# Kernel tuning notes

Hardware: AMD Instinct MI355X
Metric: run time of the kernel (lower is better)

## Reference

```python
import jax, jax.numpy as jnp
import numpy as np

NW, NT, ND = 100000, 10000, 50000
D = 128
E = {"ww": 200000, "wt": 100000, "wd": 150000, "td": 100000, "tt": 50000}


def setup_inputs() -> dict:
    key = jax.random.key(0)
    ks = iter(jax.random.split(key, 40))
    inp = {
        "h_word": jax.random.normal(next(ks), (NW, D), dtype=jnp.float32),
        "h_topic": jax.random.normal(next(ks), (NT, D), dtype=jnp.float32),
        "h_doc": jax.random.normal(next(ks), (ND, D), dtype=jnp.float32),
    }
    for et in ["ww", "wt", "wd", "td", "tt"]:
        inp[f"W_{et}"] = jax.random.normal(next(ks), (D, D), dtype=jnp.float32) * 0.05
        inp[f"b_{et}"] = jax.random.normal(next(ks), (D,), dtype=jnp.float32) * 0.05
    sizes = {"ww": (NW, NW), "wt": (NW, NT), "wd": (NW, ND), "td": (NT, ND), "tt": (NT, NT)}
    for et, (ns, nd) in sizes.items():
        inp[f"src_{et}"] = jax.random.randint(next(ks), (E[et],), 0, ns, dtype=jnp.int32)
        inp[f"dst_{et}"] = jax.random.randint(next(ks), (E[et],), 0, nd, dtype=jnp.int32)
        inp[f"ew_{et}"] = jax.random.uniform(next(ks), (E[et],), dtype=jnp.float32)
    return inp


def _linear(x, W, b):
    # torch nn.Linear: y = x @ W.T + b, W is [out, in]
    return x @ W.T + b


def _mean_agg(h_src, src, dst, ew, n_dst):
    # message m_e = h_src[src_e] * ew_e (u_mul_e), then per-dst mean (fn.mean)
    m = h_src[src] * ew[:, None]                               # [E, D]
    s = jax.ops.segment_sum(m, dst, num_segments=n_dst)        # [n_dst, D]
    cnt = jax.ops.segment_sum(jnp.ones_like(ew), dst, num_segments=n_dst)
    return s / jnp.maximum(cnt, 1.0)[:, None]


def reference(h_word, h_topic, h_doc,
              W_ww, b_ww, W_wt, b_wt, W_wd, b_wd, W_td, b_td, W_tt, b_tt,
              src_ww, dst_ww, ew_ww, src_wt, dst_wt, ew_wt,
              src_wd, dst_wd, ew_wd, src_td, dst_td, ew_td,
              src_tt, dst_tt, ew_tt):
    # DGL loop overwrites src node 'h' in-place -> linears COMPOSE per src type,
    # and messages (resolved at multi_update_all) use the final composed 'h'.
    hw = _linear(_linear(_linear(h_word, W_ww, b_ww), W_wt, b_wt), W_wd, b_wd)
    ht = _linear(_linear(h_topic, W_td, b_td), W_tt, b_tt)
    nw, nt, nd = h_word.shape[0], h_topic.shape[0], h_doc.shape[0]
    # cross-relation 'sum' of per-relation means
    out_word = _mean_agg(hw, src_ww, dst_ww, ew_ww, nw)
    out_topic = _mean_agg(hw, src_wt, dst_wt, ew_wt, nt) + _mean_agg(ht, src_tt, dst_tt, ew_tt, nt)
    out_doc = _mean_agg(hw, src_wd, dst_wd, ew_wd, nd) + _mean_agg(ht, src_td, dst_td, ew_td, nd)
    # relu + dropout (eval mode -> identity); concatenate node types for a single output
    return jnp.concatenate([
        jax.nn.relu(out_word), jax.nn.relu(out_topic), jax.nn.relu(out_doc)
    ], axis=0)
```

## Files before the change

### kernel.cpp

```cpp
#include <hip/hip_runtime.h>
#include <hip/hip_bf16.h>

#define DIM 128
#define NWORD 100000
#define NTOPIC 10000
#define NDOC 50000
#define NOUT (NWORD + NTOPIC + NDOC)

#define E_WW 200000
#define E_WT 100000
#define E_WD 150000
#define E_TD 100000
#define E_TT 50000
#define E_TOT 600000

#define B_WW 0
#define B_WT 100000
#define B_TT 110000
#define B_WD 120000
#define B_TD 170000
#define NSLOT 220000
#define NBLK_SCAN 215

typedef __attribute__((ext_vector_type(8))) short bf16x8;
typedef __attribute__((ext_vector_type(8))) unsigned short u16x8;
typedef __attribute__((ext_vector_type(4))) float f32x4;

__device__ __forceinline__ unsigned short f2bf(float f) {
    __hip_bfloat16 h = __float2bfloat16(f);
    return __builtin_bit_cast(unsigned short, h);
}
__device__ __forceinline__ float b2f(unsigned short u) {
    return __builtin_bit_cast(float, (unsigned)u << 16);
}

__global__ void compose1(const float* __restrict__ W_ww, const float* __restrict__ b_ww,
                         const float* __restrict__ W_wt, const float* __restrict__ b_wt,
                         const float* __restrict__ W_wd, const float* __restrict__ b_wd,
                         const float* __restrict__ W_td, const float* __restrict__ b_td,
                         const float* __restrict__ W_tt, const float* __restrict__ b_tt,
                         float* __restrict__ A, unsigned short* __restrict__ Wbf_t,
                         float* __restrict__ tmpb, float* __restrict__ c_t)
{
    int b = blockIdx.x, j = threadIdx.x;
    if (b < 128) {
        float s = 0.f;
        for (int m = 0; m < 128; ++m) s = fmaf(W_wd[b * 128 + m], W_wt[m * 128 + j], s);
        A[b * 128 + j] = s;
    } else if (b < 256) {
        int k = b - 128;
        float s = 0.f;
        for (int m = 0; m < 128; ++m) s = fmaf(W_tt[j * 128 + m], W_td[m * 128 + k], s);
        Wbf_t[j * 128 + k] = f2bf(s);
    } else if (b == 256) {
        float s = b_wt[j];
        for (int m = 0; m < 128; ++m) s = fmaf(W_wt[j * 128 + m], b_ww[m], s);
        tmpb[j] = s;
    } else {
        float s = b_tt[j];
        for (int m = 0; m < 128; ++m) s = fmaf(W_tt[j * 128 + m], b_td[m], s);
        c_t[j] = s;
    }
}

__global__ void compose2(const float* __restrict__ W_ww, const float* __restrict__ W_wd,
                         const float* __restrict__ b_wd, const float* __restrict__ A,
                         const float* __restrict__ tmpb,
                         unsigned short* __restrict__ Wbf_w, float* __restrict__ c_w)
{
    int b = blockIdx.x, j = threadIdx.x;
    if (b < 128) {
        int k = b;
        float s = 0.f;
        for (int m = 0; m < 128; ++m) s = fmaf(A[j * 128 + m], W_ww[m * 128 + k], s);
        Wbf_w[j * 128 + k] = f2bf(s);
    } else {
        float s = b_wd[j];
        for (int m = 0; m < 128; ++m) s = fmaf(W_wd[j * 128 + m], tmpb[m], s);
        c_w[j] = s;
    }
}

__global__ __launch_bounds__(256) void transform_mfma(
    const float* __restrict__ x, const unsigned short* __restrict__ Wbf,
    const float* __restrict__ bias, unsigned short* __restrict__ y, int ntiles)
{
    __shared__ __attribute__((aligned(16))) unsigned short xs_all[4][16 * 128];
    const int tid = threadIdx.x;
    const int wid = tid >> 6, l = tid & 63;
    char* xs = (char*)xs_all[wid];
    const int l15 = l & 15, l4 = l >> 4;

    bf16x8 wf[8][4];
#pragma unroll
    for (int cg = 0; cg < 8; ++cg)
#pragma unroll
        for (int ki = 0; ki < 4; ++ki)
            wf[cg][ki] = *(const bf16x8*)&Wbf[(cg * 16 + l15) * 128 + ki * 32 + l4 * 8];

    float bj[8];
#pragma unroll
    for (int cg = 0; cg < 8; ++cg) bj[cg] = bias[cg * 16 + l15];

    const int row_s = l >> 2, ch = l & 3;

    for (int tile = blockIdx.x * 4 + wid; tile < ntiles; tile += gridDim.x * 4) {
        const size_t rb = (size_t)tile * 16;

        const float* xr = &x[(rb + row_s) * 128 + ch * 32];
#pragma unroll
        for (int c = 0; c < 4; ++c) {
            float4 u = *(const float4*)(xr + c * 8);
            float4 v = *(const float4*)(xr + c * 8 + 4);
            u16x8 p;
            p[0] = f2bf(u.x); p[1] = f2bf(u.y); p[2] = f2bf(u.z); p[3] = f2bf(u.w);
            p[4] = f2bf(v.x); p[5] = f2bf(v.y); p[6] = f2bf(v.z); p[7] = f2bf(v.w);
            int off = row_s * 256 + ((ch * 64 + c * 16) ^ ((row_s & 7) << 4));
            *(u16x8*)(xs + off) = p;
        }

        f32x4 acc[8];
        const f32x4 zero = {0.f, 0.f, 0.f, 0.f};
#pragma unroll
        for (int cg = 0; cg < 8; ++cg) acc[cg] = zero;

#pragma unroll
        for (int ki = 0; ki < 4; ++ki) {
            int aoff = l15 * 256 + ((ki * 64 + l4 * 16) ^ ((l15 & 7) << 4));
            bf16x8 af = *(const bf16x8*)(xs + aoff);
#pragma unroll
            for (int cg = 0; cg < 8; ++cg)
                acc[cg] = __builtin_amdgcn_mfma_f32_16x16x32_bf16(af, wf[cg][ki], acc[cg], 0, 0, 0);
        }

        unsigned short* yr = &y[(rb + l4 * 4) * 128 + l15];
#pragma unroll
        for (int cg = 0; cg < 8; ++cg)
#pragma unroll
            for (int r = 0; r < 4; ++r)
                yr[r * 128 + cg * 16] = f2bf(acc[cg][r] + bj[cg]);
    }
}

__global__ void rank_count(const int* __restrict__ dst_ww, const int* __restrict__ dst_wt,
                           const int* __restrict__ dst_wd, const int* __restrict__ dst_td,
                           const int* __restrict__ dst_tt,
                           unsigned* __restrict__ cnt, unsigned* __restrict__ rank)
{
    int g = blockIdx.x * 256 + threadIdx.x;
    int slotidx;
    if (g < E_WW)                            slotidx = B_WW + dst_ww[g];
    else if (g < E_WW + E_WT)                slotidx = B_WT + dst_wt[g - E_WW];
    else if (g < E_WW + E_WT + E_WD)         slotidx = B_WD + dst_wd[g - E_WW - E_WT];
    else if (g < E_WW + E_WT + E_WD + E_TD)  slotidx = B_TD + dst_td[g - E_WW - E_WT - E_WD];
    else if (g < E_TOT)                      slotidx = B_TT + dst_tt[g - E_WW - E_WT - E_WD - E_TD];
    else return;
    rank[g] = atomicAdd(&cnt[slotidx], 1u);
}

__global__ __launch_bounds__(256) void scanA(const unsigned* __restrict__ cnt,
                                             unsigned* __restrict__ bsum)
{
    __shared__ unsigned sh[256];
    int t = threadIdx.x;
    int base = blockIdx.x * 1024 + t * 4;
    unsigned s = 0;
#pragma unroll
    for (int i = 0; i < 4; ++i) { int idx = base + i; if (idx < NSLOT) s += cnt[idx]; }
    sh[t] = s; __syncthreads();
    for (int o = 128; o > 0; o >>= 1) { if (t < o) sh[t] += sh[t + o]; __syncthreads(); }
    if (t == 0) bsum[blockIdx.x] = sh[0];
}

__global__ __launch_bounds__(256) void scanB(const unsigned* __restrict__ bsum,
                                             unsigned* __restrict__ boff)
{
    __shared__ unsigned sh[256];
    int t = threadIdx.x;
    unsigned v = (t < NBLK_SCAN) ? bsum[t] : 0u;
    sh[t] = v; __syncthreads();
    for (int o = 1; o < 256; o <<= 1) {
        unsigned x = (t >= o) ? sh[t - o] : 0u;
        __syncthreads();
        sh[t] += x;
        __syncthreads();
    }
    if (t < NBLK_SCAN) boff[t] = sh[t] - v;
}

__global__ __launch_bounds__(256) void scanC(const unsigned* __restrict__ cnt,
                                             const unsigned* __restrict__ boff,
                                             unsigned* __restrict__ offs)
{
    __shared__ unsigned sh[256];
    int t = threadIdx.x;
    int base = blockIdx.x * 1024 + t * 4;
    unsigned c[4]; unsigned s = 0;
#pragma unroll
    for (int i = 0; i < 4; ++i) {
        int idx = base + i;
        c[i] = (idx < NSLOT) ? cnt[idx] : 0u;
        s += c[i];
    }
    sh[t] = s; __syncthreads();
    for (int o = 1; o < 256; o <<= 1) {
        unsigned x = (t >= o) ? sh[t - o] : 0u;
        __syncthreads();
        sh[t] += x;
        __syncthreads();
    }
    unsigned run = boff[blockIdx.x] + sh[t] - s;
#pragma unroll
    for (int i = 0; i < 4; ++i) {
        int idx = base + i;
        if (idx < NSLOT) {
            offs[idx] = run;
            run += c[i];
            if (idx == NSLOT - 1) offs[NSLOT] = run;
        }
    }
}

__global__ void place(const int* __restrict__ dst_ww, const int* __restrict__ dst_wt,
                      const int* __restrict__ dst_wd, const int* __restrict__ dst_td,
                      const int* __restrict__ dst_tt,
                      const int* __restrict__ src_ww, const int* __restrict__ src_wt,
                      const int* __restrict__ src_wd, const int* __restrict__ src_td,
                      const int* __restrict__ src_tt,
                      const float* __restrict__ ew_ww, const float* __restrict__ ew_wt,
                      const float* __restrict__ ew_wd, const float* __restrict__ ew_td,
                      const float* __restrict__ ew_tt,
                      const unsigned* __restrict__ offs, const unsigned* __restrict__ rank,
                      uint2* __restrict__ se)
{
    int g = blockIdx.x * 256 + threadIdx.x;
    int slotidx, e; unsigned sv; float wv;
    if (g < E_WW)                            { e = g;                             slotidx = B_WW + dst_ww[e]; sv = src_ww[e]; wv = ew_ww[e]; }
    else if (g < E_WW + E_WT)                { e = g - E_WW;                      slotidx = B_WT + dst_wt[e]; sv = src_wt[e]; wv = ew_wt[e]; }
    else if (g < E_WW + E_WT + E_WD)         { e = g - E_WW - E_WT;               slotidx = B_WD + dst_wd[e]; sv = src_wd[e]; wv = ew_wd[e]; }
    else if (g < E_WW + E_WT + E_WD + E_TD)  { e = g - E_WW - E_WT - E_WD;        slotidx = B_TD + dst_td[e]; sv = src_td[e]; wv = ew_td[e]; }
    else if (g < E_TOT)                      { e = g - E_WW - E_WT - E_WD - E_TD; slotidx = B_TT + dst_tt[e]; sv = src_tt[e]; wv = ew_tt[e]; }
    else return;
    se[offs[slotidx] + rank[g]] = make_uint2(sv, __builtin_bit_cast(unsigned, wv));
}

__device__ __forceinline__ float4 seg_mean_bf(int slot,
                                              const unsigned* __restrict__ offs,
                                              const uint2* __restrict__ se,
                                              const unsigned short* __restrict__ h, int d4)
{
    unsigned off = offs[slot];
    unsigned deg = offs[slot + 1] - off;
    float ax = 0.f, ay = 0.f, az = 0.f, aw = 0.f;
    for (unsigned j = 0; j < deg; j += 4) {
        uint2 r0 = se[off + j];
        uint2 r1 = se[off + j + 1];
        uint2 r2 = se[off + j + 2];
        uint2 r3 = se[off + j + 3];
        unsigned s0 = r0.x;
        float    w0 = __builtin_bit_cast(float, r0.y);
        unsigned s1 = (j + 1 < deg) ? r1.x : 0u;
        float    w1 = (j + 1 < deg) ? __builtin_bit_cast(float, r1.y) : 0.f;
        unsigned s2 = (j + 2 < deg) ? r2.x : 0u;
        float    w2 = (j + 2 < deg) ? __builtin_bit_cast(float, r2.y) : 0.f;
        unsigned s3 = (j + 3 < deg) ? r3.x : 0u;
        float    w3 = (j + 3 < deg) ? __builtin_bit_cast(float, r3.y) : 0.f;
        ushort4 a0 = *(const ushort4*)&h[(size_t)s0 * 128 + d4];
        ushort4 a1 = *(const ushort4*)&h[(size_t)s1 * 128 + d4];
        ushort4 a2 = *(const ushort4*)&h[(size_t)s2 * 128 + d4];
        ushort4 a3 = *(const ushort4*)&h[(size_t)s3 * 128 + d4];
        ax = fmaf(b2f(a0.x), w0, ax); ay = fmaf(b2f(a0.y), w0, ay);
        az = fmaf(b2f(a0.z), w0, az); aw = fmaf(b2f(a0.w), w0, aw);
        ax = fmaf(b2f(a1.x), w1, ax); ay = fmaf(b2f(a1.y), w1, ay);
        az = fmaf(b2f(a1.z), w1, az); aw = fmaf(b2f(a1.w), w1, aw);
        ax = fmaf(b2f(a2.x), w2, ax); ay = fmaf(b2f(a2.y), w2, ay);
        az = fmaf(b2f(a2.z), w2, az); aw = fmaf(b2f(a2.w), w2, aw);
        ax = fmaf(b2f(a3.x), w3, ax); ay = fmaf(b2f(a3.y), w3, ay);
        az = fmaf(b2f(a3.z), w3, az); aw = fmaf(b2f(a3.w), w3, aw);
    }
    float inv = 1.0f / (float)(deg > 1u ? deg : 1u);
    return float4{ax * inv, ay * inv, az * inv, aw * inv};
}

__global__ void gather(const unsigned* __restrict__ offs,
                       const uint2* __restrict__ se,
                       const unsigned short* __restrict__ hw,
                       const unsigned short* __restrict__ ht,
                       float* __restrict__ out)
{
    int g = blockIdx.x * 256 + threadIdx.x;
    int n = g >> 5, d4 = (g & 31) << 2;
    if (n >= NOUT) return;
    float4 r;
    if (n < NWORD) {
        r = seg_mean_bf(B_WW + n, offs, se, hw, d4);
    } else if (n < NWORD + NTOPIC) {
        int i = n - NWORD;
        float4 a = seg_mean_bf(B_WT + i, offs, se, hw, d4);
        float4 b = seg_mean_bf(B_TT + i, offs, se, ht, d4);
        r = float4{a.x + b.x, a.y + b.y, a.z + b.z, a.w + b.w};
    } else {
        int i = n - NWORD - NTOPIC;
        float4 a = seg_mean_bf(B_WD + i, offs, se, hw, d4);
        float4 b = seg_mean_bf(B_TD + i, offs, se, ht, d4);
        r = float4{a.x + b.x, a.y + b.y, a.z + b.z, a.w + b.w};
    }
    r.x = fmaxf(r.x, 0.f); r.y = fmaxf(r.y, 0.f);
    r.z = fmaxf(r.z, 0.f); r.w = fmaxf(r.w, 0.f);
    *reinterpret_cast<float4*>(&out[(size_t)n * 128 + d4]) = r;
}

extern "C" void kernel_launch(void* const* d_in, const int* in_sizes, int n_in,
                              void* d_out, int out_size, void* d_ws, size_t ws_size,
                              hipStream_t stream) {
    const float* h_word  = (const float*)d_in[0];
    const float* h_topic = (const float*)d_in[1];
    const float* W_ww = (const float*)d_in[3];  const float* b_ww = (const float*)d_in[4];
    const float* W_wt = (const float*)d_in[5];  const float* b_wt = (const float*)d_in[6];
    const float* W_wd = (const float*)d_in[7];  const float* b_wd = (const float*)d_in[8];
    const float* W_td = (const float*)d_in[9];  const float* b_td = (const float*)d_in[10];
    const float* W_tt = (const float*)d_in[11]; const float* b_tt = (const float*)d_in[12];
    const int*   src_ww = (const int*)d_in[13]; const int* dst_ww = (const int*)d_in[14];
    const float* ew_ww  = (const float*)d_in[15];
    const int*   src_wt = (const int*)d_in[16]; const int* dst_wt = (const int*)d_in[17];
    const float* ew_wt  = (const float*)d_in[18];
    const int*   src_wd = (const int*)d_in[19]; const int* dst_wd = (const int*)d_in[20];
    const float* ew_wd  = (const float*)d_in[21];
    const int*   src_td = (const int*)d_in[22]; const int* dst_td = (const int*)d_in[23];
    const float* ew_td  = (const float*)d_in[24];
    const int*   src_tt = (const int*)d_in[25]; const int* dst_tt = (const int*)d_in[26];
    const float* ew_tt  = (const float*)d_in[27];

    float* out = (float*)d_out;

    unsigned short* hw_bf = (unsigned short*)d_ws;
    unsigned short* ht_bf = hw_bf + (size_t)NWORD * 128;
    unsigned short* Wbf_w = ht_bf + (size_t)NTOPIC * 128;
    unsigned short* Wbf_t = Wbf_w + 16384;
    float* fbase = (float*)(Wbf_t + 16384);
    float* c_w   = fbase;
    float* c_t   = c_w + 128;
    float* Amat  = c_t + 128;
    float* tmpb  = Amat + 16384;
    uint2* se    = (uint2*)(tmpb + 128);
    unsigned* cnt  = (unsigned*)(se + E_TOT + 4);
    unsigned* offs = cnt + NSLOT;
    unsigned* rank = offs + NSLOT + 1;
    unsigned* bsum = rank + E_TOT;
    unsigned* boff = bsum + 256;

    hipMemsetAsync(cnt, 0, NSLOT * sizeof(unsigned), stream);

    compose1<<<258, 128, 0, stream>>>(W_ww, b_ww, W_wt, b_wt, W_wd, b_wd, W_td, b_td,
                                      W_tt, b_tt, Amat, Wbf_t, tmpb, c_t);
    compose2<<<129, 128, 0, stream>>>(W_ww, W_wd, b_wd, Amat, tmpb, Wbf_w, c_w);

    rank_count<<<(E_TOT + 255) / 256, 256, 0, stream>>>(dst_ww, dst_wt, dst_wd, dst_td, dst_tt,
                                                        cnt, rank);
    scanA<<<NBLK_SCAN, 256, 0, stream>>>(cnt, bsum);
    scanB<<<1, 256, 0, stream>>>(bsum, boff);
    scanC<<<NBLK_SCAN, 256, 0, stream>>>(cnt, boff, offs);
    place<<<(E_TOT + 255) / 256, 256, 0, stream>>>(
        dst_ww, dst_wt, dst_wd, dst_td, dst_tt,
        src_ww, src_wt, src_wd, src_td, src_tt,
        ew_ww, ew_wt, ew_wd, ew_td, ew_tt, offs, rank, se);

    transform_mfma<<<512, 256, 0, stream>>>(h_word,  Wbf_w, c_w, hw_bf, NWORD / 16);
    transform_mfma<<<80,  256, 0, stream>>>(h_topic, Wbf_t, c_t, ht_bf, NTOPIC / 16);

    gather<<<(NOUT * 32 + 255) / 256, 256, 0, stream>>>(offs, se, hw_bf, ht_bf, out);
}
```

Before: 312.2 us.

## Fuse prep kernels, merge word/topic transforms, and prefetch next tile input

Folds the memset of the count array into the first compose kernel and merges rank_count into the second compose kernel, removing two launches. The two transform_mfma launches become one grid that splits blocks between word and topic work. Inside the transform loop, the next tile's fp32 input is loaded into registers before the current tile's MFMAs run, to overlap global loads with compute. The compose loops also gain four independent accumulators for more ILP, at the cost of higher register use and a slightly different fp32 summation order.

```diff
diff --git a/kernel.cpp b/kernel.cpp
--- a/kernel.cpp
+++ b/kernel.cpp
@@ -22,6 +22,9 @@
 #define NSLOT 220000
 #define NBLK_SCAN 215
 
+#define NBW 512
+#define NBT 64
+
 typedef __attribute__((ext_vector_type(8))) short bf16x8;
 typedef __attribute__((ext_vector_type(8))) unsigned short u16x8;
 typedef __attribute__((ext_vector_type(4))) float f32x4;
@@ -34,24 +37,39 @@
     return __builtin_bit_cast(float, (unsigned)u << 16);
 }
 
-__global__ void compose1(const float* __restrict__ W_ww, const float* __restrict__ b_ww,
-                         const float* __restrict__ W_wt, const float* __restrict__ b_wt,
-                         const float* __restrict__ W_wd, const float* __restrict__ b_wd,
-                         const float* __restrict__ W_td, const float* __restrict__ b_td,
-                         const float* __restrict__ W_tt, const float* __restrict__ b_tt,
-                         float* __restrict__ A, unsigned short* __restrict__ Wbf_t,
-                         float* __restrict__ tmpb, float* __restrict__ c_t)
+__global__ __launch_bounds__(128) void prep1(
+    const float* __restrict__ W_ww, const float* __restrict__ b_ww,
+    const float* __restrict__ W_wt, const float* __restrict__ b_wt,
+    const float* __restrict__ W_wd, const float* __restrict__ b_wd,
+    const float* __restrict__ W_td, const float* __restrict__ b_td,
+    const float* __restrict__ W_tt, const float* __restrict__ b_tt,
+    float* __restrict__ A, unsigned short* __restrict__ Wbf_t,
+    float* __restrict__ tmpb, float* __restrict__ c_t, unsigned* __restrict__ cnt)
 {
     int b = blockIdx.x, j = threadIdx.x;
+    for (int i = b * 128 + j; i < NSLOT; i += gridDim.x * 128) cnt[i] = 0u;
+
     if (b < 128) {
-        float s = 0.f;
-        for (int m = 0; m < 128; ++m) s = fmaf(W_wd[b * 128 + m], W_wt[m * 128 + j], s);
-        A[b * 128 + j] = s;
+        const float* wr = &W_wd[b * 128];
+        float s0 = 0.f, s1 = 0.f, s2 = 0.f, s3 = 0.f;
+        for (int m = 0; m < 128; m += 4) {
+            s0 = fmaf(wr[m + 0], W_wt[(m + 0) * 128 + j], s0);
+            s1 = fmaf(wr[m + 1], W_wt[(m + 1) * 128 + j], s1);
+            s2 = fmaf(wr[m + 2], W_wt[(m + 2) * 128 + j], s2);
+            s3 = fmaf(wr[m + 3], W_wt[(m + 3) * 128 + j], s3);
+        }
+        A[b * 128 + j] = (s0 + s1) + (s2 + s3);
     } else if (b < 256) {
         int k = b - 128;
-        float s = 0.f;
-        for (int m = 0; m < 128; ++m) s = fmaf(W_tt[j * 128 + m], W_td[m * 128 + k], s);
-        Wbf_t[j * 128 + k] = f2bf(s);
+        const float* wr = &W_tt[j * 128];
+        float s0 = 0.f, s1 = 0.f, s2 = 0.f, s3 = 0.f;
+        for (int m = 0; m < 128; m += 4) {
+            s0 = fmaf(wr[m + 0], W_td[(m + 0) * 128 + k], s0);
+            s1 = fmaf(wr[m + 1], W_td[(m + 1) * 128 + k], s1);
+            s2 = fmaf(wr[m + 2], W_td[(m + 2) * 128 + k], s2);
+            s3 = fmaf(wr[m + 3], W_td[(m + 3) * 128 + k], s3);
+        }
+        Wbf_t[j * 128 + k] = f2bf((s0 + s1) + (s2 + s3));
     } else if (b == 256) {
         float s = b_wt[j];
         for (int m = 0; m < 128; ++m) s = fmaf(W_wt[j * 128 + m], b_ww[m], s);
@@ -63,27 +81,52 @@
     }
 }
 
-__global__ void compose2(const float* __restrict__ W_ww, const float* __restrict__ W_wd,
-                         const float* __restrict__ b_wd, const float* __restrict__ A,
-                         const float* __restrict__ tmpb,
-                         unsigned short* __restrict__ Wbf_w, float* __restrict__ c_w)
-{
-    int b = blockIdx.x, j = threadIdx.x;
-    if (b < 128) {
-        int k = b;
-        float s = 0.f;
-        for (int m = 0; m < 128; ++m) s = fmaf(A[j * 128 + m], W_ww[m * 128 + k], s);
-        Wbf_w[j * 128 + k] = f2bf(s);
+__global__ __launch_bounds__(256) void prep2(
+    const float* __restrict__ W_ww, const float* __restrict__ W_wd,
+    const float* __restrict__ b_wd, const float* __restrict__ A,
+    const float* __restrict__ tmpb,
+    unsigned short* __restrict__ Wbf_w, float* __restrict__ c_w,
+    const int* __restrict__ dst_ww, const int* __restrict__ dst_wt,
+    const int* __restrict__ dst_wd, const int* __restrict__ dst_td,
+    const int* __restrict__ dst_tt,
+    unsigned* __restrict__ cnt, unsigned* __restrict__ rank)
+{
+    int b = blockIdx.x, tid = threadIdx.x;
+    if (b < 64) {
+        int k = b * 2 + (tid >> 7), j = tid & 127;
+        const float* ar = &A[j * 128];
+        float s0 = 0.f, s1 = 0.f, s2 = 0.f, s3 = 0.f;
+        for (int m = 0; m < 128; m += 4) {
+            s0 = fmaf(ar[m + 0], W_ww[(m + 0) * 128 + k], s0);
+            s1 = fmaf(ar[m + 1], W_ww[(m + 1) * 128 + k], s1);
+            s2 = fmaf(ar[m + 2], W_ww[(m + 2) * 128 + k], s2);
+            s3 = fmaf(ar[m + 3], W_ww[(m + 3) * 128 + k], s3);
+        }
+        Wbf_w[j * 128 + k] = f2bf((s0 + s1) + (s2 + s3));
+    } else if (b == 64) {
+        if (tid < 128) {
+            float s = b_wd[tid];
+            for (int m = 0; m < 128; ++m) s = fmaf(W_wd[tid * 128 + m], tmpb[m], s);
+            c_w[tid] = s;
+        }
     } else {
-        float s = b_wd[j];
-        for (int m = 0; m < 128; ++m) s = fmaf(W_wd[j * 128 + m], tmpb[m], s);
-        c_w[j] = s;
+        int g = (b - 65) * 256 + tid;
+        int slotidx;
+        if (g < E_WW)                            slotidx = B_WW + dst_ww[g];
+        else if (g < E_WW + E_WT)                slotidx = B_WT + dst_wt[g - E_WW];
+        else if (g < E_WW + E_WT + E_WD)         slotidx = B_WD + dst_wd[g - E_WW - E_WT];
+        else if (g < E_WW + E_WT + E_WD + E_TD)  slotidx = B_TD + dst_td[g - E_WW - E_WT - E_WD];
+        else if (g < E_TOT)                      slotidx = B_TT + dst_tt[g - E_WW - E_WT - E_WD - E_TD];
+        else return;
+        rank[g] = atomicAdd(&cnt[slotidx], 1u);
     }
 }
 
 __global__ __launch_bounds__(256) void transform_mfma(
-    const float* __restrict__ x, const unsigned short* __restrict__ Wbf,
-    const float* __restrict__ bias, unsigned short* __restrict__ y, int ntiles)
+    const float* __restrict__ xw, const unsigned short* __restrict__ Wbf_w,
+    const float* __restrict__ cw, unsigned short* __restrict__ yw, int ntw,
+    const float* __restrict__ xt, const unsigned short* __restrict__ Wbf_t,
+    const float* __restrict__ ct, unsigned short* __restrict__ yt, int ntt)
 {
     __shared__ __attribute__((aligned(16))) unsigned short xs_all[4][16 * 128];
     const int tid = threadIdx.x;
@@ -91,6 +134,15 @@
     char* xs = (char*)xs_all[wid];
     const int l15 = l & 15, l4 = l >> 4;
 
+    const bool isw = blockIdx.x < NBW;
+    const float* x = isw ? xw : xt;
+    const unsigned short* Wbf = isw ? Wbf_w : Wbf_t;
+    const float* bias = isw ? cw : ct;
+    unsigned short* y = isw ? yw : yt;
+    const int nt = isw ? ntw : ntt;
+    const int t0 = (isw ? blockIdx.x : blockIdx.x - NBW) * 4 + wid;
+    const int tstr = (isw ? NBW : NBT) * 4;
+
     bf16x8 wf[8][4];
 #pragma unroll
     for (int cg = 0; cg < 8; ++cg)
@@ -104,19 +156,27 @@
 
     const int row_s = l >> 2, ch = l & 3;
 
-    for (int tile = blockIdx.x * 4 + wid; tile < ntiles; tile += gridDim.x * 4) {
-        const size_t rb = (size_t)tile * 16;
-
-        const float* xr = &x[(rb + row_s) * 128 + ch * 32];
+    float4 u[4], v[4];
+    if (t0 < nt) {
+        const float* xr = &x[((size_t)t0 * 16 + row_s) * 128 + ch * 32];
+#pragma unroll
+        for (int c = 0; c < 4; ++c) { u[c] = *(const float4*)(xr + c * 8); v[c] = *(const float4*)(xr + c * 8 + 4); }
+    }
+
+    for (int tile = t0; tile < nt; tile += tstr) {
 #pragma unroll
         for (int c = 0; c < 4; ++c) {
-            float4 u = *(const float4*)(xr + c * 8);
-            float4 v = *(const float4*)(xr + c * 8 + 4);
             u16x8 p;
-            p[0] = f2bf(u.x); p[1] = f2bf(u.y); p[2] = f2bf(u.z); p[3] = f2bf(u.w);
-            p[4] = f2bf(v.x); p[5] = f2bf(v.y); p[6] = f2bf(v.z); p[7] = f2bf(v.w);
+            p[0] = f2bf(u[c].x); p[1] = f2bf(u[c].y); p[2] = f2bf(u[c].z); p[3] = f2bf(u[c].w);
+            p[4] = f2bf(v[c].x); p[5] = f2bf(v[c].y); p[6] = f2bf(v[c].z); p[7] = f2bf(v[c].w);
             int off = row_s * 256 + ((ch * 64 + c * 16) ^ ((row_s & 7) << 4));
             *(u16x8*)(xs + off) = p;
+        }
+        int nxt = tile + tstr;
+        if (nxt < nt) {
+            const float* xr = &x[((size_t)nxt * 16 + row_s) * 128 + ch * 32];
+#pragma unroll
+            for (int c = 0; c < 4; ++c) { u[c] = *(const float4*)(xr + c * 8); v[c] = *(const float4*)(xr + c * 8 + 4); }
         }
 
         f32x4 acc[8];
@@ -133,29 +193,13 @@
                 acc[cg] = __builtin_amdgcn_mfma_f32_16x16x32_bf16(af, wf[cg][ki], acc[cg], 0, 0, 0);
         }
 
-        unsigned short* yr = &y[(rb + l4 * 4) * 128 + l15];
+        unsigned short* yr = &y[((size_t)tile * 16 + l4 * 4) * 128 + l15];
 #pragma unroll
         for (int cg = 0; cg < 8; ++cg)
 #pragma unroll
             for (int r = 0; r < 4; ++r)
                 yr[r * 128 + cg * 16] = f2bf(acc[cg][r] + bj[cg]);
     }
-}
-
-__global__ void rank_count(const int* __restrict__ dst_ww, const int* __restrict__ dst_wt,
-                           const int* __restrict__ dst_wd, const int* __restrict__ dst_td,
-                           const int* __restrict__ dst_tt,
-                           unsigned* __restrict__ cnt, unsigned* __restrict__ rank)
-{
-    int g = blockIdx.x * 256 + threadIdx.x;
-    int slotidx;
-    if (g < E_WW)                            slotidx = B_WW + dst_ww[g];
-    else if (g < E_WW + E_WT)                slotidx = B_WT + dst_wt[g - E_WW];
-    else if (g < E_WW + E_WT + E_WD)         slotidx = B_WD + dst_wd[g - E_WW - E_WT];
-    else if (g < E_WW + E_WT + E_WD + E_TD)  slotidx = B_TD + dst_td[g - E_WW - E_WT - E_WD];
-    else if (g < E_TOT)                      slotidx = B_TT + dst_tt[g - E_WW - E_WT - E_WD - E_TD];
-    else return;
-    rank[g] = atomicAdd(&cnt[slotidx], 1u);
 }
 
 __global__ __launch_bounds__(256) void scanA(const unsigned* __restrict__ cnt,
@@ -349,14 +393,12 @@
     unsigned* bsum = rank + E_TOT;
     unsigned* boff = bsum + 256;
 
-    hipMemsetAsync(cnt, 0, NSLOT * sizeof(unsigned), stream);
-
-    compose1<<<258, 128, 0, stream>>>(W_ww, b_ww, W_wt, b_wt, W_wd, b_wd, W_td, b_td,
-                                      W_tt, b_tt, Amat, Wbf_t, tmpb, c_t);
-    compose2<<<129, 128, 0, stream>>>(W_ww, W_wd, b_wd, Amat, tmpb, Wbf_w, c_w);
-
-    rank_count<<<(E_TOT + 255) / 256, 256, 0, stream>>>(dst_ww, dst_wt, dst_wd, dst_td, dst_tt,
-                                                        cnt, rank);
+    prep1<<<258, 128, 0, stream>>>(W_ww, b_ww, W_wt, b_wt, W_wd, b_wd, W_td, b_td,
+                                   W_tt, b_tt, Amat, Wbf_t, tmpb, c_t, cnt);
+    prep2<<<65 + (E_TOT + 255) / 256, 256, 0, stream>>>(
+        W_ww, W_wd, b_wd, Amat, tmpb, Wbf_w, c_w,
+        dst_ww, dst_wt, dst_wd, dst_td, dst_tt, cnt, rank);
+
     scanA<<<NBLK_SCAN, 256, 0, stream>>>(cnt, bsum);
     scanB<<<1, 256, 0, stream>>>(bsum, boff);
     scanC<<<NBLK_SCAN, 256, 0, stream>>>(cnt, boff, offs);
@@ -365,8 +407,9 @@
         src_ww, src_wt, src_wd, src_td, src_tt,
         ew_ww, ew_wt, ew_wd, ew_td, ew_tt, offs, rank, se);
 
-    transform_mfma<<<512, 256, 0, stream>>>(h_word,  Wbf_w, c_w, hw_bf, NWORD / 16);
-    transform_mfma<<<80,  256, 0, stream>>>(h_topic, Wbf_t, c_t, ht_bf, NTOPIC / 16);
+    transform_mfma<<<NBW + NBT, 256, 0, stream>>>(
+        h_word,  Wbf_w, c_w, hw_bf, NWORD / 16,
+        h_topic, Wbf_t, c_t, ht_bf, NTOPIC / 16);
 
     gather<<<(NOUT * 32 + 255) / 256, 256, 0, stream>>>(offs, se, hw_bf, ht_bf, out);
 }
```

Result: faster. 301.3 us (-3.5%).
